# Performance work log

Measured on AMD Instinct MI355X. Metric: run time of the kernel, lower is better.

The kernel has to match this reference:

```python
import jax, jax.numpy as jnp
import numpy as np

DATA_NUM = 1024
CLS_NUM = 32000


def setup_inputs() -> dict:
    key = jax.random.key(0)
    k1, k2, k3, k4 = jax.random.split(key, 4)
    h1 = jax.random.normal(k1, (DATA_NUM, 2), dtype=jnp.float32) + 3.0
    e1 = jax.random.normal(k2, (CLS_NUM, 2), dtype=jnp.float32)
    h3 = jax.random.normal(k3, (DATA_NUM, 2), dtype=jnp.float32) * 2.0
    e3 = jax.random.normal(k4, (CLS_NUM, 2), dtype=jnp.float32)
    return {"h1": h1, "e1": e1, "h3": h3, "e3": e3, "share_head": 0}


def cal_akl(l1, l2):
    # l1: student logits (D, C); l2: teacher logits (D, C)
    probs1 = jax.nn.softmax(l1, axis=-1)
    probs2 = jax.nn.softmax(l2, axis=-1)
    # sort teacher probs ascending; gather student probs in same order
    sorted_idx = jnp.argsort(probs2, axis=-1)
    sorted_probs2 = jnp.take_along_axis(probs2, sorted_idx, axis=-1)
    sorted_probs1 = jnp.take_along_axis(probs1, sorted_idx, axis=-1)
    gap = jnp.abs(sorted_probs2 - sorted_probs1)
    cum_probs2 = jnp.cumsum(sorted_probs2, axis=-1)
    tail_mask = (cum_probs2 < 0.5).astype(l1.dtype)
    g_head = jax.lax.stop_gradient(jnp.sum(gap * (1.0 - tail_mask), axis=-1))
    g_tail = jax.lax.stop_gradient(jnp.sum(gap * tail_mask, axis=-1))
    lprobs1 = jax.nn.log_softmax(l1, axis=-1)
    lprobs2 = jax.nn.log_softmax(l2, axis=-1)
    fkl = jnp.sum(probs2 * (lprobs2 - lprobs1), axis=-1)
    rkl = jnp.sum(probs1 * (lprobs1 - lprobs2), axis=-1)
    denom = g_head + g_tail
    akl = (g_head / denom) * fkl + (g_tail / denom) * rkl
    return jnp.mean(akl)


def reference(h1, e1, h3, e3, share_head):
    # share_head is a static Python int/bool; obj == 'akl', share_head == 0 path
    if share_head:
        raise NotImplementedError("reference covers share_head=False path")
    stu_logits = h1 @ e1.T   # (D, C)
    tea_logits = h3 @ e3.T   # (D, C)
    return cal_akl(stu_logits, tea_logits)
```

## Files before the change

kernel.cpp:

```cpp
#include <hip/hip_runtime.h>
#include <math.h>

#define DNUM 1024
#define CNUM 32000
#define NT 512
#define GRID DNUM
#define KC 4
#define KF 8
#define NQ (CNUM / 4)
#define NFULL (NQ / NT)
#define TAILN (NQ - NFULL*NT)

#define L2E 1.4426950408889634f
#define LN2 0.6931471805599453f

typedef float v2f __attribute__((ext_vector_type(2)));

__device__ __forceinline__ v2f splat2(float s) { v2f v; v.x = s; v.y = s; return v; }

__device__ __forceinline__ float wave_red_sum(float v) {
    #pragma unroll
    for (int o = 32; o > 0; o >>= 1) v += __shfl_down(v, o, 64);
    return v;
}

__global__ __launch_bounds__(NT, 8) void akl_rows(
    const float* __restrict__ h1, const float* __restrict__ e1,
    const float* __restrict__ h3, const float* __restrict__ e3,
    float* __restrict__ out)
{
    const int tid  = threadIdx.x;
    const int lane = tid & 63, wid = tid >> 6;
    const int row = blockIdx.x;

    __shared__ float pool[8192];
    __shared__ float red[24];
    __shared__ float shCS[KC];
    __shared__ float shFP[KF], shFG[KF];
    __shared__ float shA[7];

    const float a1L = h1[2*row] * L2E,  b1L = h1[2*row+1] * L2E;
    const float a2L = h3[2*row] * L2E,  b2L = h3[2*row+1] * L2E;
    const float mh1L = 6.0f * (fabsf(a1L) + fabsf(b1L));
    const float mh2L = 6.0f * (fabsf(a2L) + fabsf(b2L));
    const float spC = fmaxf(sqrtf(a2L*a2L + b2L*b2L), 1e-6f);
    const float icwC = 1.0f / (1.35f * spC);
    const float c0C = 0.5f/1.35f + mh2L*icwC;

    for (int i = tid; i < 8192; i += NT) pool[i] = 0.f;
    __syncthreads();

    const float4* __restrict__ E1 = (const float4*)e1;
    const float4* __restrict__ E3 = (const float4*)e3;

    const int cnt = NFULL + ((tid < TAILN) ? 1 : 0);

    v2f U1v = splat2(0.f), S1v = splat2(0.f), S2v = splat2(0.f);

    {
        const v2f a1v = splat2(a1L), b1v = splat2(b1L);
        const v2f a2v = splat2(a2L), b2v = splat2(b2L);
        const v2f m1v = splat2(-mh1L), m2v = splat2(-mh2L);
        const v2f icv = splat2(icwC), c0v = splat2(c0C);
        #pragma unroll 1
        for (int it = 0; it < cnt; ++it) {
            const int j = it*NT + tid;
            float4 A0 = E1[2*j], A1 = E1[2*j+1];
            float4 B0 = E3[2*j], B1 = E3[2*j+1];
            #pragma unroll
            for (int p = 0; p < 2; p++) {
                float4 A = p ? A1 : A0, B = p ? B1 : B0;
                v2f X1; X1.x = A.x; X1.y = A.z;
                v2f Y1; Y1.x = A.y; Y1.y = A.w;
                v2f X3; X3.x = B.x; X3.y = B.z;
                v2f Y3; Y3.x = B.y; Y3.y = B.w;
                v2f l1 = a1v*X1 + (b1v*Y1 + m1v);
                v2f l2 = a2v*X3 + (b2v*Y3 + m2v);
                v2f e1v; e1v.x = __builtin_amdgcn_exp2f(l1.x);
                         e1v.y = __builtin_amdgcn_exp2f(l1.y);
                v2f e2v; e2v.x = __builtin_amdgcn_exp2f(l2.x);
                         e2v.y = __builtin_amdgcn_exp2f(l2.y);
                v2f dp = l2 - l1;
                U1v += e1v;
                S1v += e1v * dp;
                S2v += e2v * dp;
                v2f t = l2*icv + c0v;
                float t0 = fminf(fmaxf(t.x, 0.f), 3.f);
                float t1 = fminf(fmaxf(t.y, 0.f), 3.f);
                int b0 = (int)t0, b1i = (int)t1;
                float* H0 = pool + (2*p    )*2048;
                float* H1 = pool + (2*p + 1)*2048;
                H0[b0*NT + tid]  += e2v.x;
                H1[b1i*NT + tid] += e2v.y;
            }
        }
    }

    {
        float u  = wave_red_sum(U1v.x + U1v.y);
        float s1 = wave_red_sum(S1v.x + S1v.y);
        float s2 = wave_red_sum(S2v.x + S2v.y);
        if (lane == 0) {
            red[wid*3 + 0] = u;
            red[wid*3 + 1] = s1;
            red[wid*3 + 2] = s2;
        }
    }
    __syncthreads();

    if (tid < 256) {
        int b = tid >> 6, l = tid & 63;
        float s = 0.f;
        #pragma unroll
        for (int c = 0; c < 4; c++) {
            const float* H = pool + c*2048 + b*512;
            #pragma unroll
            for (int t = 0; t < 8; t++) s += H[l + t*64];
        }
        s = wave_red_sum(s);
        if (l == 0) shCS[b] = s;
    }
    __syncthreads();

    if (tid == 0) {
        float U1s = 0, S1s = 0, S2s = 0;
        for (int w = 0; w < 8; w++) {
            U1s += red[w*3 + 0];
            S1s += red[w*3 + 1];
            S2s += red[w*3 + 2];
        }
        float U2s = 0.f;
        #pragma unroll
        for (int i = 0; i < KC; i++) U2s += shCS[i];
        float dmh = mh2L - mh1L;
        S1s += dmh * U1s;
        S2s += dmh * U2s;
        float M1 = mh1L + __builtin_amdgcn_logf(U1s);
        float M2 = mh2L + __builtin_amdgcn_logf(U2s);
        float delta = M2 - M1;
        float thr = 0.5f * U2s;
        float S = 0.f; int bsel = KC-1;
        for (int i = 0; i < KC; i++) {
            float m = shCS[i];
            if (S + m >= thr) { bsel = i; break; }
            S += m;
        }
        float wc  = 1.35f * spC;
        float loS_s = fmaf((float)bsel, wc, -0.5f*spC) - mh2L;
        float icwF = (float)KF / wc;
        shA[0] = U2s / U1s;
        shA[1] = thr;
        shA[2] = LN2 * (S2s/U2s - delta);
        shA[3] = LN2 * (delta - S1s/U1s);
        shA[4] = icwF;
        shA[5] = -loS_s * icwF;
        shA[6] = S;
    }
    for (int i = tid; i < 8192; i += NT) pool[i] = 0.f;
    __syncthreads();

    const float cR = shA[0], icwF = shA[4], c0F = shA[5];
    v2f gtv = splat2(0.f), Gpv = splat2(0.f);

    {
        const v2f a1v = splat2(a1L), b1v = splat2(b1L);
        const v2f a2v = splat2(a2L), b2v = splat2(b2L);
        const v2f m1v = splat2(-mh1L), m2v = splat2(-mh2L);
        const v2f cv = splat2(-cR);
        const v2f icv = splat2(icwF), c0v = splat2(c0F);
        float* HP = pool;
        float* HG = pool + 4096;
        #pragma unroll 1
        for (int it = 0; it < cnt; ++it) {
            const int j = it*NT + tid;
            float4 A0 = E1[2*j], A1 = E1[2*j+1];
            float4 B0 = E3[2*j], B1 = E3[2*j+1];
            #pragma unroll
            for (int p = 0; p < 2; p++) {
                float4 A = p ? A1 : A0, B = p ? B1 : B0;
                v2f X1; X1.x = A.x; X1.y = A.z;
                v2f Y1; Y1.x = A.y; Y1.y = A.w;
                v2f X3; X3.x = B.x; X3.y = B.z;
                v2f Y3; Y3.x = B.y; Y3.y = B.w;
                v2f l1 = a1v*X1 + (b1v*Y1 + m1v);
                v2f l2 = a2v*X3 + (b2v*Y3 + m2v);
                v2f e1v; e1v.x = __builtin_amdgcn_exp2f(l1.x);
                         e1v.y = __builtin_amdgcn_exp2f(l1.y);
                v2f e2v; e2v.x = __builtin_amdgcn_exp2f(l2.x);
                         e2v.y = __builtin_amdgcn_exp2f(l2.y);
                v2f d = cv*e1v + e2v;
                v2f gap; gap.x = fabsf(d.x); gap.y = fabsf(d.y);
                gtv += gap;
                v2f t = l2*icv + c0v;
                Gpv.x += (t.x < 0.f) ? gap.x : 0.f;
                Gpv.y += (t.y < 0.f) ? gap.y : 0.f;
                if (t.x >= 0.f && t.x < (float)KF) {
                    int fb = (int)t.x;
                    HP[fb*NT + tid] += e2v.x;
                    HG[fb*NT + tid] += gap.x;
                }
                if (t.y >= 0.f && t.y < (float)KF) {
                    int fb = (int)t.y;
                    HP[fb*NT + tid] += e2v.y;
                    HG[fb*NT + tid] += gap.y;
                }
            }
        }
    }

    {
        float a = wave_red_sum(gtv.x + gtv.y);
        float b = wave_red_sum(Gpv.x + Gpv.y);
        if (lane == 0) { red[wid*2 + 0] = a; red[wid*2 + 1] = b; }
    }
    __syncthreads();

    {
        int grp = tid >> 5, l32 = tid & 31;
        int isG = grp >> 3, b = grp & 7;
        const float* H = pool + isG*4096 + b*512;
        float s = 0.f;
        #pragma unroll
        for (int t = 0; t < NT/32; t++) s += H[l32 + t*32];
        #pragma unroll
        for (int o = 16; o > 0; o >>= 1) s += __shfl_down(s, o, 32);
        if (l32 == 0) {
            if (isG) shFG[b] = s; else shFP[b] = s;
        }
    }
    __syncthreads();

    if (tid == 0) {
        float gts = 0, Gp = 0;
        for (int w = 0; w < 8; w++) {
            gts += red[w*2 + 0];
            Gp  += red[w*2 + 1];
        }
        float thr = shA[1], fkl = shA[2], rkl = shA[3];
        float S = shA[6], G = Gp;
        bool done = false;
        #pragma unroll
        for (int i = 0; i < KF; i++) {
            if (!done) {
                float p = shFP[i], g = shFG[i];
                float ns = S + p;
                if (ns >= thr) {
                    float f = (thr - S) / fmaxf(p, 1e-30f);
                    f = fminf(fmaxf(f, 0.f), 1.f);
                    G += f * g;
                    done = true;
                } else { S = ns; G += g; }
            }
        }
        float gl = G;
        float gh = gts - gl;
        float akl = (gh*fkl + gl*rkl) / gts;
        unsafeAtomicAdd(out, akl * (1.0f/(float)DNUM));
    }
}

extern "C" void kernel_launch(void* const* d_in, const int* in_sizes, int n_in,
                              void* d_out, int out_size, void* d_ws, size_t ws_size,
                              hipStream_t stream) {
    const float* h1 = (const float*)d_in[0];
    const float* e1 = (const float*)d_in[1];
    const float* h3 = (const float*)d_in[2];
    const float* e3 = (const float*)d_in[3];
    hipMemsetAsync(d_out, 0, sizeof(float), stream);
    akl_rows<<<GRID, NT, 0, stream>>>(h1, e1, h3, e3, (float*)d_out);
}
```

Measured before the change: 110.3 us.

## Replace coarse LDS histogram with power-moment sums and prefetch next tile loads

```diff
diff --git a/kernel.cpp b/kernel.cpp
--- a/kernel.cpp
+++ b/kernel.cpp
@@ -34,8 +34,7 @@
     const int row = blockIdx.x;
 
     __shared__ float pool[8192];
-    __shared__ float red[24];
-    __shared__ float shCS[KC];
+    __shared__ float red[56];
     __shared__ float shFP[KF], shFG[KF];
     __shared__ float shA[7];
 
@@ -47,29 +46,29 @@
     const float icwC = 1.0f / (1.35f * spC);
     const float c0C = 0.5f/1.35f + mh2L*icwC;
 
-    for (int i = tid; i < 8192; i += NT) pool[i] = 0.f;
-    __syncthreads();
-
     const float4* __restrict__ E1 = (const float4*)e1;
     const float4* __restrict__ E3 = (const float4*)e3;
 
     const int cnt = NFULL + ((tid < TAILN) ? 1 : 0);
 
     v2f U1v = splat2(0.f), S1v = splat2(0.f), S2v = splat2(0.f);
+    v2f q0v = splat2(0.f), q1v = splat2(0.f), q2v = splat2(0.f), q3v = splat2(0.f);
 
     {
         const v2f a1v = splat2(a1L), b1v = splat2(b1L);
         const v2f a2v = splat2(a2L), b2v = splat2(b2L);
         const v2f m1v = splat2(-mh1L), m2v = splat2(-mh2L);
         const v2f icv = splat2(icwC), c0v = splat2(c0C);
+        float4 cA0 = E1[2*tid], cA1 = E1[2*tid+1];
+        float4 cB0 = E3[2*tid], cB1 = E3[2*tid+1];
         #pragma unroll 1
         for (int it = 0; it < cnt; ++it) {
-            const int j = it*NT + tid;
-            float4 A0 = E1[2*j], A1 = E1[2*j+1];
-            float4 B0 = E3[2*j], B1 = E3[2*j+1];
+            const int jn = (it+1 < cnt) ? ((it+1)*NT + tid) : tid;
+            float4 nA0 = E1[2*jn], nA1 = E1[2*jn+1];
+            float4 nB0 = E3[2*jn], nB1 = E3[2*jn+1];
             #pragma unroll
             for (int p = 0; p < 2; p++) {
-                float4 A = p ? A1 : A0, B = p ? B1 : B0;
+                float4 A = p ? cA1 : cA0, B = p ? cB1 : cB0;
                 v2f X1; X1.x = A.x; X1.y = A.z;
                 v2f Y1; Y1.x = A.y; Y1.y = A.w;
                 v2f X3; X3.x = B.x; X3.y = B.z;
@@ -85,53 +84,53 @@
                 S1v += e1v * dp;
                 S2v += e2v * dp;
                 v2f t = l2*icv + c0v;
-                float t0 = fminf(fmaxf(t.x, 0.f), 3.f);
-                float t1 = fminf(fmaxf(t.y, 0.f), 3.f);
-                int b0 = (int)t0, b1i = (int)t1;
-                float* H0 = pool + (2*p    )*2048;
-                float* H1 = pool + (2*p + 1)*2048;
-                H0[b0*NT + tid]  += e2v.x;
-                H1[b1i*NT + tid] += e2v.y;
+                v2f bfv;
+                bfv.x = truncf(fminf(fmaxf(t.x, 0.f), 3.f));
+                bfv.y = truncf(fminf(fmaxf(t.y, 0.f), 3.f));
+                v2f bf2 = bfv*bfv, bf3 = bf2*bfv;
+                q0v += e2v;
+                q1v += e2v * bfv;
+                q2v += e2v * bf2;
+                q3v += e2v * bf3;
             }
-        }
-    }
-
-    {
-        float u  = wave_red_sum(U1v.x + U1v.y);
-        float s1 = wave_red_sum(S1v.x + S1v.y);
-        float s2 = wave_red_sum(S2v.x + S2v.y);
+            cA0 = nA0; cA1 = nA1; cB0 = nB0; cB1 = nB1;
+        }
+    }
+
+    {
+        float v0 = wave_red_sum(U1v.x + U1v.y);
+        float v1 = wave_red_sum(S1v.x + S1v.y);
+        float v2 = wave_red_sum(S2v.x + S2v.y);
+        float v3 = wave_red_sum(q0v.x + q0v.y);
+        float v4 = wave_red_sum(q1v.x + q1v.y);
+        float v5 = wave_red_sum(q2v.x + q2v.y);
+        float v6 = wave_red_sum(q3v.x + q3v.y);
         if (lane == 0) {
-            red[wid*3 + 0] = u;
-            red[wid*3 + 1] = s1;
-            red[wid*3 + 2] = s2;
-        }
-    }
-    __syncthreads();
-
-    if (tid < 256) {
-        int b = tid >> 6, l = tid & 63;
-        float s = 0.f;
-        #pragma unroll
-        for (int c = 0; c < 4; c++) {
-            const float* H = pool + c*2048 + b*512;
-            #pragma unroll
-            for (int t = 0; t < 8; t++) s += H[l + t*64];
-        }
-        s = wave_red_sum(s);
-        if (l == 0) shCS[b] = s;
-    }
+            red[wid*7 + 0] = v0; red[wid*7 + 1] = v1; red[wid*7 + 2] = v2;
+            red[wid*7 + 3] = v3; red[wid*7 + 4] = v4; red[wid*7 + 5] = v5;
+            red[wid*7 + 6] = v6;
+        }
+    }
+    for (int i = tid; i < 8192; i += NT) pool[i] = 0.f;
     __syncthreads();
 
     if (tid == 0) {
-        float U1s = 0, S1s = 0, S2s = 0;
+        float U1s = 0, S1s = 0, S2s = 0, Q0 = 0, Q1 = 0, Q2 = 0, Q3 = 0;
         for (int w = 0; w < 8; w++) {
-            U1s += red[w*3 + 0];
-            S1s += red[w*3 + 1];
-            S2s += red[w*3 + 2];
-        }
-        float U2s = 0.f;
-        #pragma unroll
-        for (int i = 0; i < KC; i++) U2s += shCS[i];
+            U1s += red[w*7 + 0];
+            S1s += red[w*7 + 1];
+            S2s += red[w*7 + 2];
+            Q0  += red[w*7 + 3];
+            Q1  += red[w*7 + 4];
+            Q2  += red[w*7 + 5];
+            Q3  += red[w*7 + 6];
+        }
+        float U2s = Q0;
+        float sb[KC];
+        sb[0] = Q0 - (11.f*Q1 - 6.f*Q2 + Q3) * (1.f/6.f);
+        sb[1] = (6.f*Q1 - 5.f*Q2 + Q3) * 0.5f;
+        sb[2] = (4.f*Q2 - 3.f*Q1 - Q3) * 0.5f;
+        sb[3] = (2.f*Q1 - 3.f*Q2 + Q3) * (1.f/6.f);
         float dmh = mh2L - mh1L;
         S1s += dmh * U1s;
         S2s += dmh * U2s;
@@ -141,7 +140,7 @@
         float thr = 0.5f * U2s;
         float S = 0.f; int bsel = KC-1;
         for (int i = 0; i < KC; i++) {
-            float m = shCS[i];
+            float m = sb[i];
             if (S + m >= thr) { bsel = i; break; }
             S += m;
         }
@@ -156,7 +155,6 @@
         shA[5] = -loS_s * icwF;
         shA[6] = S;
     }
-    for (int i = tid; i < 8192; i += NT) pool[i] = 0.f;
     __syncthreads();
 
     const float cR = shA[0], icwF = shA[4], c0F = shA[5];
@@ -170,14 +168,16 @@
         const v2f icv = splat2(icwF), c0v = splat2(c0F);
         float* HP = pool;
         float* HG = pool + 4096;
+        float4 cA0 = E1[2*tid], cA1 = E1[2*tid+1];
+        float4 cB0 = E3[2*tid], cB1 = E3[2*tid+1];
         #pragma unroll 1
         for (int it = 0; it < cnt; ++it) {
-            const int j = it*NT + tid;
-            float4 A0 = E1[2*j], A1 = E1[2*j+1];
-            float4 B0 = E3[2*j], B1 = E3[2*j+1];
+            const int jn = (it+1 < cnt) ? ((it+1)*NT + tid) : tid;
+            float4 nA0 = E1[2*jn], nA1 = E1[2*jn+1];
+            float4 nB0 = E3[2*jn], nB1 = E3[2*jn+1];
             #pragma unroll
             for (int p = 0; p < 2; p++) {
-                float4 A = p ? A1 : A0, B = p ? B1 : B0;
+                float4 A = p ? cA1 : cA0, B = p ? cB1 : cB0;
                 v2f X1; X1.x = A.x; X1.y = A.z;
                 v2f Y1; Y1.x = A.y; Y1.y = A.w;
                 v2f X3; X3.x = B.x; X3.y = B.z;
@@ -205,6 +205,7 @@
                     HG[fb*NT + tid] += gap.y;
                 }
             }
+            cA0 = nA0; cA1 = nA1; cB0 = nB0; cB1 = nB1;
         }
     }
 
```

Result: slower. 116.9 us (+5.9%).
